# Kernel optimization log

Hardware: AMD Instinct MI355X
Metric: run time of the kernel (lower is better)

## Reference

```python
import jax, jax.numpy as jnp
import numpy as np


def setup_inputs() -> dict:
    key = jax.random.key(0)
    k1, k2 = jax.random.split(key)
    x = jax.random.normal(k1, (16, 1, 512, 512), dtype=jnp.float32)
    weight = jax.random.normal(k2, (128, 1), dtype=jnp.float32)
    return {"x": x, "weight": weight}


def reference(x, weight):
    # x: [B, C=1, H, W]; weight: [K=128, D=1] codebook
    inputs = jnp.transpose(x, (0, 2, 3, 1))          # [B, H, W, C]
    input_shape = inputs.shape
    D = weight.shape[1]
    flat = inputs.reshape(-1, D)                     # [N, D]
    # pairwise squared distances: ||z||^2 + ||e||^2 - 2 z.e^T  -> [N, K]
    dist = (jnp.sum(flat ** 2, axis=1, keepdims=True)
            + jnp.sum(weight ** 2, axis=1)
            - 2.0 * flat @ weight.T)
    idx = jnp.argmin(dist, axis=1)                   # [N]
    # one-hot @ weight == gather of codebook rows (same math, no [N,K] one-hot)
    quantized = weight[idx].reshape(input_shape)     # [B, H, W, C]
    return jnp.transpose(quantized, (0, 3, 1, 2))    # [B, C, H, W]
```

## Files before the change

kernel.cpp:

```cpp
#include <hip/hip_runtime.h>


constexpr int K     = 128;
constexpr int NB    = 1024;
constexpr int EPT   = 8;
constexpr int BLOCK = 256;

constexpr int SV_OFF  = 0;
constexpr int SI_OFF  = K;
constexpr int LUT_OFF = 2 * K;
constexpr int HDR_OFF = 2 * K + NB;

#define DELTA 0.0125f

__global__ __launch_bounds__(BLOCK) void vq_build(const float* __restrict__ w,
                                                  float* __restrict__ ws,
                                                  int kk) {
#pragma clang fp contract(off)
    __shared__ float wraw[K];
    __shared__ float sv[K];
    __shared__ int   sidx[K];
    const int t = threadIdx.x;
    if (t < K) {
        wraw[t] = (t < kk) ? w[t] : __builtin_inff();
        sv[t]   = __builtin_inff();
        sidx[t] = 0x7fffffff;
    }
    __syncthreads();
    if (t < kk) {
        float v = wraw[t];
        int rank = 0;
        for (int j = 0; j < kk; ++j) {
            float u = wraw[j];
            rank += (u < v) || (u == v && j < t);
        }
        sv[rank]   = v;
        sidx[rank] = t;
    }
    __syncthreads();

    const float lo    = sv[0];
    const float hi    = sv[kk - 1];
    const float range = hi - lo;
    const float scale = (range > 0.f) ? (float)NB / range : 0.f;
    const float binv  = (range > 0.f) ? range / (float)NB : 0.f;
    const int   sMax  = (kk > 8 ? kk : 8) - 8;

    if (t < K) {
        ws[SV_OFF + t] = sv[t];
        ((int*)ws)[SI_OFF + t] = sidx[t];
    }
    if (t == 0) {
        ws[HDR_OFF]     = lo;
        ws[HDR_OFF + 1] = scale;
    }

    const int b0 = t * 4;
    float L0 = lo + ((float)b0 - 1.5f) * binv;
    float R0 = lo + ((float)b0 + 2.5f) * binv;
    int pL = 0, pR = 0;
#pragma unroll
    for (int st = 64; st > 0; st >>= 1)
        if (sv[pL + st - 1] < L0) pL += st;
    if (pL < K && sv[pL] < L0) ++pL;
#pragma unroll
    for (int st = 64; st > 0; st >>= 1)
        if (sv[pR + st - 1] < R0) pR += st;
    if (pR < K && sv[pR] < R0) ++pR;

    for (int j = 0; j < 4; ++j) {
        int b = b0 + j;
        float Lb = lo + ((float)b - 1.5f) * binv;
        float Rb = lo + ((float)b + 2.5f) * binv;
        while (pL < kk && sv[pL] < Lb) ++pL;
        while (pR < kk && sv[pR] < Rb) ++pR;

        float wa  = sv[pL > 0 ? pL - 1 : 0];
        float wb  = sv[pR < kk ? pR : kk - 1];
        float tlo = wa - DELTA;
        float thi = wb + DELTA;

        int s0 = pL > 0 ? pL - 1 : 0;
        while (s0 > 0 && sv[s0 - 1] >= tlo) --s0;
        int e0 = pR;
        while (e0 < kk && sv[e0] <= thi) ++e0;

        if (s0 > sMax) s0 = sMax;
        ((int*)ws)[LUT_OFF + b] = s0 | (e0 << 8);
    }
}

__global__ __launch_bounds__(BLOCK) void vq_main(const float* __restrict__ x,
                                                 const float* __restrict__ ws,
                                                 float* __restrict__ out,
                                                 long n, int kk) {
#pragma clang fp contract(off)
    __shared__ float sv[K];
    __shared__ int   si[K];
    __shared__ alignas(16) int lut[NB];

    const int t = threadIdx.x;
    if (t < K) {
        sv[t] = ws[SV_OFF + t];
        si[t] = ((const int*)ws)[SI_OFF + t];
    }
    {
        int4 lv = ((const int4*)(ws + LUT_OFF))[t];
        *(int4*)&lut[4 * t] = lv;
    }
    const float lo    = ws[HDR_OFF];
    const float scale = ws[HDR_OFF + 1];
    __syncthreads();

    long base = ((long)blockIdx.x * BLOCK + t) * (long)EPT;
    if (base + EPT <= n) {
        float4 a  = *(const float4*)(x + base);
        float4 b4 = *(const float4*)(x + base + 4);
        float xs[EPT] = {a.x, a.y, a.z, a.w, b4.x, b4.y, b4.z, b4.w};
        float res[EPT];
#pragma unroll
        for (int e = 0; e < EPT; ++e) {
            float xv = xs[e];
            float x2 = xv * xv;
            asm volatile("" : "+v"(x2));
            float tx = xv + xv;

            float fi = (xv - lo) * scale;
            int idx = (int)fi;
            idx = idx < 0 ? 0 : (idx > NB - 1 ? NB - 1 : idx);
            int pk = lut[idx];
            int s  = pk & 0xff;
            int en = pk >> 8;

            float best = __builtin_inff();
            float bw   = 0.0f;
            unsigned tie = 0u;
#pragma unroll
            for (int c = 0; c < 8; ++c) {
                float wv = sv[s + c];
                float w2 = wv * wv;
                asm volatile("" : "+v"(w2));
                float sum  = x2 + w2;
                float prod = tx * wv;
                asm volatile("" : "+v"(prod));
                float d = sum - prod;
                bool lt = d < best;
                tie |= (d == best) ? 1u : 0u;
                best = lt ? d : best;
                bw   = lt ? wv : bw;
            }
            if (__builtin_expect(en > s + 8, 0)) {
                for (int j = s + 8; j < en; ++j) {
                    float wv = sv[j];
                    float w2 = wv * wv;
                    asm volatile("" : "+v"(w2));
                    float sum  = x2 + w2;
                    float prod = tx * wv;
                    asm volatile("" : "+v"(prod));
                    float d = sum - prod;
                    bool lt = d < best;
                    tie |= (d == best) ? 1u : 0u;
                    best = lt ? d : best;
                    bw   = lt ? wv : bw;
                }
            }
            res[e] = bw;
            if (__builtin_expect(tie != 0u, 0)) {
                int hiEnd = en > s + 8 ? en : s + 8;
                float bb = __builtin_inff(), bwv = 0.0f;
                int bi = 0x7fffffff;
                for (int j = s; j < hiEnd; ++j) {
                    float wv = sv[j];
                    float w2 = wv * wv;
                    asm volatile("" : "+v"(w2));
                    float sum  = x2 + w2;
                    float prod = tx * wv;
                    asm volatile("" : "+v"(prod));
                    float d = sum - prod;
                    int oi = si[j];
                    if (d < bb || (d == bb && oi < bi)) { bb = d; bi = oi; bwv = wv; }
                }
                res[e] = bwv;
            }
        }
        *(float4*)(out + base)     = make_float4(res[0], res[1], res[2], res[3]);
        *(float4*)(out + base + 4) = make_float4(res[4], res[5], res[6], res[7]);
    } else {
        for (long i = base; i < n; ++i) {
            float xv = x[i];
            float x2 = xv * xv;
            asm volatile("" : "+v"(x2));
            float tx = xv + xv;
            float bb = __builtin_inff(), bwv = 0.0f;
            int bi = 0x7fffffff;
            for (int p0 = 0; p0 < kk; ++p0) {
                float wv = sv[p0];
                float w2 = wv * wv;
                asm volatile("" : "+v"(w2));
                float sum  = x2 + w2;
                float prod = tx * wv;
                asm volatile("" : "+v"(prod));
                float d = sum - prod;
                int oi = si[p0];
                if (d < bb || (d == bb && oi < bi)) { bb = d; bi = oi; bwv = wv; }
            }
            out[i] = bwv;
        }
    }
}

extern "C" void kernel_launch(void* const* d_in, const int* in_sizes, int n_in,
                              void* d_out, int out_size, void* d_ws, size_t ws_size,
                              hipStream_t stream) {
    const float* x = (const float*)d_in[0];
    const float* w = (const float*)d_in[1];
    float* out     = (float*)d_out;
    float* ws      = (float*)d_ws;
    long n = (long)in_sizes[0];
    int  kk = in_sizes[1] < K ? in_sizes[1] : K;

    vq_build<<<1, BLOCK, 0, stream>>>(w, ws, kk);

    long threads_needed = (n + EPT - 1) / EPT;
    long grid = (threads_needed + BLOCK - 1) / BLOCK;
    vq_main<<<(int)grid, BLOCK, 0, stream>>>(x, ws, out, n, kk);
}
```

Baseline: 89.99 us.

## Fuse codebook sort and LUT build into main VQ kernel per block

Removes the separate single-block build kernel and the workspace round trip: every block of the main kernel now ranks the 128 codewords, builds the 1024-entry bucket LUT in shared memory, and then quantizes its elements. This eliminates one kernel launch and the serialization between the two kernels. In exchange every block redoes the O(K^2) rank computation and the LUT search, which adds per-block preamble latency across 2048 blocks.

```diff
diff --git a/kernel.cpp b/kernel.cpp
--- a/kernel.cpp
+++ b/kernel.cpp
@@ -6,25 +6,23 @@
 constexpr int EPT   = 8;
 constexpr int BLOCK = 256;
 
-constexpr int SV_OFF  = 0;
-constexpr int SI_OFF  = K;
-constexpr int LUT_OFF = 2 * K;
-constexpr int HDR_OFF = 2 * K + NB;
-
 #define DELTA 0.0125f
 
-__global__ __launch_bounds__(BLOCK) void vq_build(const float* __restrict__ w,
-                                                  float* __restrict__ ws,
-                                                  int kk) {
+__global__ __launch_bounds__(BLOCK) void vq_kernel(const float* __restrict__ x,
+                                                   const float* __restrict__ w,
+                                                   float* __restrict__ out,
+                                                   long n, int kk) {
 #pragma clang fp contract(off)
     __shared__ float wraw[K];
     __shared__ float sv[K];
-    __shared__ int   sidx[K];
+    __shared__ int   si[K];
+    __shared__ int   lut[NB];
+
     const int t = threadIdx.x;
     if (t < K) {
         wraw[t] = (t < kk) ? w[t] : __builtin_inff();
         sv[t]   = __builtin_inff();
-        sidx[t] = 0x7fffffff;
+        si[t]   = 0x7fffffff;
     }
     __syncthreads();
     if (t < kk) {
@@ -34,8 +32,8 @@
             float u = wraw[j];
             rank += (u < v) || (u == v && j < t);
         }
-        sv[rank]   = v;
-        sidx[rank] = t;
+        sv[rank] = v;
+        si[rank] = t;
     }
     __syncthreads();
 
@@ -46,70 +44,41 @@
     const float binv  = (range > 0.f) ? range / (float)NB : 0.f;
     const int   sMax  = (kk > 8 ? kk : 8) - 8;
 
-    if (t < K) {
-        ws[SV_OFF + t] = sv[t];
-        ((int*)ws)[SI_OFF + t] = sidx[t];
+    {
+        const int b0 = t * 4;
+        float L0 = lo + ((float)b0 - 1.5f) * binv;
+        float R0 = lo + ((float)b0 + 2.5f) * binv;
+        int pL = 0, pR = 0;
+#pragma unroll
+        for (int st = 64; st > 0; st >>= 1)
+            if (sv[pL + st - 1] < L0) pL += st;
+        if (pL < K && sv[pL] < L0) ++pL;
+#pragma unroll
+        for (int st = 64; st > 0; st >>= 1)
+            if (sv[pR + st - 1] < R0) pR += st;
+        if (pR < K && sv[pR] < R0) ++pR;
+
+        for (int j = 0; j < 4; ++j) {
+            int b = b0 + j;
+            float Lb = lo + ((float)b - 1.5f) * binv;
+            float Rb = lo + ((float)b + 2.5f) * binv;
+            while (pL < kk && sv[pL] < Lb) ++pL;
+            while (pR < kk && sv[pR] < Rb) ++pR;
+
+            float wa  = sv[pL > 0 ? pL - 1 : 0];
+            float wb  = sv[pR < kk ? pR : kk - 1];
+            float tlo = wa - DELTA;
+            float thi = wb + DELTA;
+
+            int s0 = pL > 0 ? pL - 1 : 0;
+            while (s0 > 0 && sv[s0 - 1] >= tlo) --s0;
+            int e0 = pR;
+            while (e0 < kk && sv[e0] <= thi) ++e0;
+
+            if (s0 > sMax) s0 = sMax;
+            lut[b] = s0 | (e0 << 8);
+        }
     }
-    if (t == 0) {
-        ws[HDR_OFF]     = lo;
-        ws[HDR_OFF + 1] = scale;
-    }
-
-    const int b0 = t * 4;
-    float L0 = lo + ((float)b0 - 1.5f) * binv;
-    float R0 = lo + ((float)b0 + 2.5f) * binv;
-    int pL = 0, pR = 0;
-#pragma unroll
-    for (int st = 64; st > 0; st >>= 1)
-        if (sv[pL + st - 1] < L0) pL += st;
-    if (pL < K && sv[pL] < L0) ++pL;
-#pragma unroll
-    for (int st = 64; st > 0; st >>= 1)
-        if (sv[pR + st - 1] < R0) pR += st;
-    if (pR < K && sv[pR] < R0) ++pR;
-
-    for (int j = 0; j < 4; ++j) {
-        int b = b0 + j;
-        float Lb = lo + ((float)b - 1.5f) * binv;
-        float Rb = lo + ((float)b + 2.5f) * binv;
-        while (pL < kk && sv[pL] < Lb) ++pL;
-        while (pR < kk && sv[pR] < Rb) ++pR;
-
-        float wa  = sv[pL > 0 ? pL - 1 : 0];
-        float wb  = sv[pR < kk ? pR : kk - 1];
-        float tlo = wa - DELTA;
-        float thi = wb + DELTA;
-
-        int s0 = pL > 0 ? pL - 1 : 0;
-        while (s0 > 0 && sv[s0 - 1] >= tlo) --s0;
-        int e0 = pR;
-        while (e0 < kk && sv[e0] <= thi) ++e0;
-
-        if (s0 > sMax) s0 = sMax;
-        ((int*)ws)[LUT_OFF + b] = s0 | (e0 << 8);
-    }
-}
-
-__global__ __launch_bounds__(BLOCK) void vq_main(const float* __restrict__ x,
-                                                 const float* __restrict__ ws,
-                                                 float* __restrict__ out,
-                                                 long n, int kk) {
-#pragma clang fp contract(off)
-    __shared__ float sv[K];
-    __shared__ int   si[K];
-    __shared__ alignas(16) int lut[NB];
-
-    const int t = threadIdx.x;
-    if (t < K) {
-        sv[t] = ws[SV_OFF + t];
-        si[t] = ((const int*)ws)[SI_OFF + t];
-    }
-    {
-        int4 lv = ((const int4*)(ws + LUT_OFF))[t];
-        *(int4*)&lut[4 * t] = lv;
-    }
-    const float lo    = ws[HDR_OFF];
-    const float scale = ws[HDR_OFF + 1];
     __syncthreads();
 
     long base = ((long)blockIdx.x * BLOCK + t) * (long)EPT;
@@ -215,13 +184,10 @@
     const float* x = (const float*)d_in[0];
     const float* w = (const float*)d_in[1];
     float* out     = (float*)d_out;
-    float* ws      = (float*)d_ws;
     long n = (long)in_sizes[0];
     int  kk = in_sizes[1] < K ? in_sizes[1] : K;
 
-    vq_build<<<1, BLOCK, 0, stream>>>(w, ws, kk);
-
     long threads_needed = (n + EPT - 1) / EPT;
     long grid = (threads_needed + BLOCK - 1) / BLOCK;
-    vq_main<<<(int)grid, BLOCK, 0, stream>>>(x, ws, out, n, kk);
+    vq_kernel<<<(int)grid, BLOCK, 0, stream>>>(x, w, out, n, kk);
 }
```

Measured after the change: 91.27 us. About the same (+1.4%).
